# Performance work log

Measured on AMD Instinct MI355X. Metric: run time of the kernel, lower is better.

The kernel has to match this reference:

```python
import jax, jax.numpy as jnp
import numpy as np
from jax import lax

N_EMBD = 4096
N_EXPERTS = 64


def setup_inputs() -> dict:
    key = jax.random.key(0)
    kx, kw = jax.random.split(key)
    x = jax.random.normal(kx, (4, 4096, N_EMBD), dtype=jnp.float32)
    # nn.Linear(n_embd, n_experts, bias=False) -> weight shape [n_experts, n_embd]
    W = jax.random.normal(kw, (N_EXPERTS, N_EMBD), dtype=jnp.float32) * (1.0 / np.sqrt(N_EMBD))
    return {"x": x, "W": W}


def reference(x, W):
    # logits = x @ W^T : [B, S, n_experts]
    logits = jnp.einsum('bsd,ed->bse', x, W)
    topk_vals, topk_idx = lax.top_k(logits, 2)  # [B, S, 2]
    gates = jax.nn.softmax(topk_vals, axis=-1)  # softmax over just the top-2 values
    return (topk_idx, gates)
```

## Files before the change

kernel.cpp:

```cpp
#include <hip/hip_runtime.h>
#include <math.h>

#define N_EMBD    4096
#define N_EXPERTS 64
#define N_TOKENS  16384
#define TAU       1e-3f
#define BM        16
#define BK        128
#define NTILES    (N_EMBD / BK)

typedef __attribute__((ext_vector_type(8))) short bf16x8;
typedef __attribute__((ext_vector_type(4))) float f32x4;

#define MFMA16 __builtin_amdgcn_mfma_f32_16x16x32_bf16

struct hl_pair { unsigned h, l; };

__device__ __forceinline__ hl_pair split_pair(float f0, float f1) {
    unsigned u0 = __builtin_bit_cast(unsigned, f0);
    unsigned u1 = __builtin_bit_cast(unsigned, f1);
    unsigned r0 = u0 + 0x7FFFu + ((u0 >> 16) & 1u);
    unsigned r1 = u1 + 0x7FFFu + ((u1 >> 16) & 1u);
    hl_pair p;
    p.h = (r0 >> 16) | (r1 & 0xFFFF0000u);
    float h0 = __builtin_bit_cast(float, r0 & 0xFFFF0000u);
    float h1 = __builtin_bit_cast(float, r1 & 0xFFFF0000u);
    float l0 = f0 - h0;
    float l1 = f1 - h1;
    unsigned v0 = __builtin_bit_cast(unsigned, l0);
    unsigned v1 = __builtin_bit_cast(unsigned, l1);
    unsigned s0 = v0 + 0x7FFFu + ((v0 >> 16) & 1u);
    unsigned s1 = v1 + 0x7FFFu + ((v1 >> 16) & 1u);
    p.l = (s0 >> 16) | (s1 & 0xFFFF0000u);
    return p;
}

__global__ void w_pack_bf16(const float* __restrict__ W,
                            uint4* __restrict__ Bpack,
                            int* __restrict__ flags) {
    int tid = blockIdx.x * blockDim.x + threadIdx.x;
    if (tid == 0) flags[0] = 0;
    int lane = tid & 63;
    int nt   = (tid >> 6) & 3;
    int ks   = tid >> 8;
    int e = nt * 16 + (lane & 15);
    int k = ks * 32 + ((lane >> 4) << 3);
    const float* src = W + (size_t)e * N_EMBD + k;
    uint4 hp, lp;
    hl_pair p0 = split_pair(src[0], src[1]);
    hl_pair p1 = split_pair(src[2], src[3]);
    hl_pair p2 = split_pair(src[4], src[5]);
    hl_pair p3 = split_pair(src[6], src[7]);
    hp.x = p0.h; lp.x = p0.l;
    hp.y = p1.h; lp.y = p1.l;
    hp.z = p2.h; lp.z = p2.l;
    hp.w = p3.h; lp.w = p3.l;
    size_t F = (size_t)ks * 8 + nt * 2;
    Bpack[F * 64 + lane]       = hp;
    Bpack[(F + 1) * 64 + lane] = lp;
}

__device__ __forceinline__ void store_split(char* ldsA, int off, f32x4 v) {
    hl_pair p01 = split_pair(v.x, v.y);
    hl_pair p23 = split_pair(v.z, v.w);
    uint2 hw, lw;
    hw.x = p01.h; hw.y = p23.h;
    lw.x = p01.l; lw.y = p23.l;
    *(uint2*)(ldsA + off)        = hw;
    *(uint2*)(ldsA + off + 4096) = lw;
}

__global__ __launch_bounds__(256, 3) void router_fused(
        const float* __restrict__ x,
        const uint4* __restrict__ Bpack,
        float* __restrict__ out,
        int* __restrict__ flags) {
    __shared__ __align__(16) char ldsA[8192];
    __shared__ float red[BM][64];

    const int tid  = threadIdx.x;
    const int lane = tid & 63;
    const int w    = tid >> 6;
    const int tok0 = blockIdx.x * BM;

    const int k4   = tid & 31;
    const int row0 = tid >> 5;
    const f32x4* g0 = (const f32x4*)x + (size_t)(tok0 + row0) * (N_EMBD / 4) + k4;
    const f32x4* g1 = g0 + 8 * (N_EMBD / 4);
    const int swz = (row0 & 7) << 4;
    const int wo0 = ((row0    ) * 256 + k4 * 8) ^ swz;
    const int wo1 = ((row0 + 8) * 256 + k4 * 8) ^ swz;

    const int l15 = lane & 15, l16 = lane >> 4;
    const int ro_base = l15 * 256 + l16 * 16;
    const int swz_r   = (l15 & 7) << 4;

    f32x4 acc = {0.f, 0.f, 0.f, 0.f};

    f32x4 r0 = g0[0];
    f32x4 r1 = g1[0];
    for (int t = 0; t < NTILES; ++t) {
        __syncthreads();
        store_split(ldsA, wo0, r0);
        store_split(ldsA, wo1, r1);
        if (t + 1 < NTILES) {
            r0 = g0[(t + 1) * (BK / 4)];
            r1 = g1[(t + 1) * (BK / 4)];
        }
        __syncthreads();
#pragma unroll
        for (int ksl = 0; ksl < 4; ++ksl) {
            const uint4* bq = Bpack + ((size_t)(t * 4 + ksl) * 8 + w * 2) * 64 + lane;
            uint4 bhq = bq[0];
            uint4 blq = bq[64];
            const int off = (ro_base + ksl * 64) ^ swz_r;
            bf16x8 ah = *(const bf16x8*)(ldsA + off);
            bf16x8 al = *(const bf16x8*)(ldsA + off + 4096);
            bf16x8 bh = __builtin_bit_cast(bf16x8, bhq);
            bf16x8 bl = __builtin_bit_cast(bf16x8, blq);
            acc = MFMA16(ah, bh, acc, 0, 0, 0);
            acc = MFMA16(ah, bl, acc, 0, 0, 0);
            acc = MFMA16(al, bh, acc, 0, 0, 0);
        }
    }

    const int rb = l16 << 2;
#pragma unroll
    for (int j = 0; j < 4; ++j)
        red[rb + j][w * 16 + l15] = acc[j];
    __syncthreads();

    for (int tt = 0; tt < 4; ++tt) {
        const int t = w * 4 + tt;
        float v = red[t][lane];

        float m1 = v; int i1 = lane;
#pragma unroll
        for (int off = 32; off; off >>= 1) {
            float ov = __shfl_xor(m1, off); int oi = __shfl_xor(i1, off);
            if (ov > m1 || (ov == m1 && oi < i1)) { m1 = ov; i1 = oi; }
        }
        float m2 = (lane == i1) ? -INFINITY : v; int i2 = lane;
#pragma unroll
        for (int off = 32; off; off >>= 1) {
            float ov = __shfl_xor(m2, off); int oi = __shfl_xor(i2, off);
            if (ov > m2 || (ov == m2 && oi < i2)) { m2 = ov; i2 = oi; }
        }
        float m3 = (lane == i1 || lane == i2) ? -INFINITY : v;
#pragma unroll
        for (int off = 32; off; off >>= 1)
            m3 = fmaxf(m3, __shfl_xor(m3, off));

        if (lane == 0) {
            const int tok = tok0 + t;
            float e2  = __expf(m2 - m1);
            float inv = 1.0f / (1.0f + e2);
            float2 idx = make_float2((float)i1, (float)i2);
            float2 gts = make_float2(inv, e2 * inv);
            *(float2*)(out + 2 * tok) = idx;
            *(float2*)(out + 2 * N_TOKENS + 2 * tok) = gts;
            if ((m1 - m2 < TAU) || (m2 - m3 < TAU)) {
                int p = atomicAdd(flags, 1);
                if (p < N_TOKENS) flags[1 + p] = tok;
            }
        }
    }
}

__global__ __launch_bounds__(256) void refine(const float* __restrict__ x,
                                              const float* __restrict__ W,
                                              const int* __restrict__ flags,
                                              float* __restrict__ out) {
    __shared__ double redd[64];
    const int lane = threadIdx.x & 63;
    const int wv   = threadIdx.x >> 6;
    int cnt = flags[0];
    if (cnt > N_TOKENS) cnt = N_TOKENS;

    for (int i = blockIdx.x; i < cnt; i += gridDim.x) {
        const int tok = flags[1 + i];
        const float4* xr4 = (const float4*)(x + (size_t)tok * N_EMBD);
#pragma unroll
        for (int ee = 0; ee < 16; ++ee) {
            const int e = wv * 16 + ee;
            const float4* wr = (const float4*)(W + (size_t)e * N_EMBD);
            double acc = 0.0;
#pragma unroll 4
            for (int c = 0; c < 16; ++c) {
                float4 xv = xr4[c * 64 + lane];
                float4 wq = wr[c * 64 + lane];
                acc += (double)xv.x * wq.x + (double)xv.y * wq.y
                     + (double)xv.z * wq.z + (double)xv.w * wq.w;
            }
#pragma unroll
            for (int off = 32; off; off >>= 1)
                acc += __shfl_xor(acc, off);
            if (lane == 0) redd[e] = acc;
        }
        __syncthreads();
        if (wv == 0) {
            double v = redd[lane];
            double m1 = v; int i1 = lane;
#pragma unroll
            for (int off = 32; off; off >>= 1) {
                double ov = __shfl_xor(m1, off); int oi = __shfl_xor(i1, off);
                if (ov > m1 || (ov == m1 && oi < i1)) { m1 = ov; i1 = oi; }
            }
            double m2 = (lane == i1) ? -INFINITY : v; int i2 = lane;
#pragma unroll
            for (int off = 32; off; off >>= 1) {
                double ov = __shfl_xor(m2, off); int oi = __shfl_xor(i2, off);
                if (ov > m2 || (ov == m2 && oi < i2)) { m2 = ov; i2 = oi; }
            }
            if (lane == 0) {
                double e2  = exp(m2 - m1);
                double inv = 1.0 / (1.0 + e2);
                out[2 * tok + 0] = (float)i1;
                out[2 * tok + 1] = (float)i2;
                out[2 * N_TOKENS + 2 * tok + 0] = (float)inv;
                out[2 * N_TOKENS + 2 * tok + 1] = (float)(e2 * inv);
            }
        }
        __syncthreads();
    }
}

extern "C" void kernel_launch(void* const* d_in, const int* in_sizes, int n_in,
                              void* d_out, int out_size, void* d_ws, size_t ws_size,
                              hipStream_t stream) {
    const float* x = (const float*)d_in[0];
    const float* W = (const float*)d_in[1];
    float* out = (float*)d_out;

    uint4* Bpack = (uint4*)d_ws;
    int*   flags = (int*)((char*)d_ws + (2u << 20));

    w_pack_bf16 <<<128, 256, 0, stream>>>(W, Bpack, flags);
    router_fused<<<N_TOKENS / BM, 256, 0, stream>>>(x, Bpack, out, flags);
    refine      <<<128, 256, 0, stream>>>(x, W, flags, out);
}
```

Measured before the change: 110.8 us.

## Double-buffer LDS A tiles with one barrier per K step and deeper prefetch

Switches the A-tile staging in LDS to double buffering, so each K iteration needs one barrier instead of two. Global loads of x are now issued two tiles ahead, and all four B fragments per tile are loaded up front before the MFMAs. The occupancy hint rises from 3 to 4 blocks per CU. The cost is twice the LDS per block and more live registers, which may work against the higher occupancy target.

```diff
diff --git a/kernel.cpp b/kernel.cpp
--- a/kernel.cpp
+++ b/kernel.cpp
@@ -60,22 +60,22 @@
     Bpack[(F + 1) * 64 + lane] = lp;
 }
 
-__device__ __forceinline__ void store_split(char* ldsA, int off, f32x4 v) {
+__device__ __forceinline__ void store_split(char* buf, int off, f32x4 v) {
     hl_pair p01 = split_pair(v.x, v.y);
     hl_pair p23 = split_pair(v.z, v.w);
     uint2 hw, lw;
     hw.x = p01.h; hw.y = p23.h;
     lw.x = p01.l; lw.y = p23.l;
-    *(uint2*)(ldsA + off)        = hw;
-    *(uint2*)(ldsA + off + 4096) = lw;
-}
-
-__global__ __launch_bounds__(256, 3) void router_fused(
+    *(uint2*)(buf + off)        = hw;
+    *(uint2*)(buf + off + 4096) = lw;
+}
+
+__global__ __launch_bounds__(256, 4) void router_fused(
         const float* __restrict__ x,
         const uint4* __restrict__ Bpack,
         float* __restrict__ out,
         int* __restrict__ flags) {
-    __shared__ __align__(16) char ldsA[8192];
+    __shared__ __align__(16) char ldsA[2 * 8192];
     __shared__ float red[BM][64];
 
     const int tid  = threadIdx.x;
@@ -94,33 +94,65 @@
     const int l15 = lane & 15, l16 = lane >> 4;
     const int ro_base = l15 * 256 + l16 * 16;
     const int swz_r   = (l15 & 7) << 4;
+    const int off0 = (ro_base +   0) ^ swz_r;
+    const int off1 = (ro_base +  64) ^ swz_r;
+    const int off2 = (ro_base + 128) ^ swz_r;
+    const int off3 = (ro_base + 192) ^ swz_r;
 
     f32x4 acc = {0.f, 0.f, 0.f, 0.f};
 
     f32x4 r0 = g0[0];
     f32x4 r1 = g1[0];
+    store_split(ldsA, wo0, r0);
+    store_split(ldsA, wo1, r1);
+    r0 = g0[BK / 4];
+    r1 = g1[BK / 4];
+    asm volatile("s_waitcnt lgkmcnt(0)" ::: "memory");
+    __builtin_amdgcn_s_barrier();
+    __builtin_amdgcn_sched_barrier(0);
+
     for (int t = 0; t < NTILES; ++t) {
-        __syncthreads();
-        store_split(ldsA, wo0, r0);
-        store_split(ldsA, wo1, r1);
+        char* bufr = ldsA + (t & 1) * 8192;
+        char* bufw = ldsA + ((t & 1) ^ 1) * 8192;
+
+        const uint4* bq = Bpack + ((size_t)(t * 4) * 8 + w * 2) * 64 + lane;
+        uint4 bh0 = bq[0];    uint4 bl0 = bq[64];
+        uint4 bh1 = bq[512];  uint4 bl1 = bq[576];
+        uint4 bh2 = bq[1024]; uint4 bl2 = bq[1088];
+        uint4 bh3 = bq[1536]; uint4 bl3 = bq[1600];
+
+        bf16x8 ah, al;
+        ah = *(const bf16x8*)(bufr + off0);
+        al = *(const bf16x8*)(bufr + off0 + 4096);
+        acc = MFMA16(ah, __builtin_bit_cast(bf16x8, bh0), acc, 0, 0, 0);
+        acc = MFMA16(ah, __builtin_bit_cast(bf16x8, bl0), acc, 0, 0, 0);
+        acc = MFMA16(al, __builtin_bit_cast(bf16x8, bh0), acc, 0, 0, 0);
+        ah = *(const bf16x8*)(bufr + off1);
+        al = *(const bf16x8*)(bufr + off1 + 4096);
+        acc = MFMA16(ah, __builtin_bit_cast(bf16x8, bh1), acc, 0, 0, 0);
+        acc = MFMA16(ah, __builtin_bit_cast(bf16x8, bl1), acc, 0, 0, 0);
+        acc = MFMA16(al, __builtin_bit_cast(bf16x8, bh1), acc, 0, 0, 0);
+        ah = *(const bf16x8*)(bufr + off2);
+        al = *(const bf16x8*)(bufr + off2 + 4096);
+        acc = MFMA16(ah, __builtin_bit_cast(bf16x8, bh2), acc, 0, 0, 0);
+        acc = MFMA16(ah, __builtin_bit_cast(bf16x8, bl2), acc, 0, 0, 0);
+        acc = MFMA16(al, __builtin_bit_cast(bf16x8, bh2), acc, 0, 0, 0);
+        ah = *(const bf16x8*)(bufr + off3);
+        al = *(const bf16x8*)(bufr + off3 + 4096);
+        acc = MFMA16(ah, __builtin_bit_cast(bf16x8, bh3), acc, 0, 0, 0);
+        acc = MFMA16(ah, __builtin_bit_cast(bf16x8, bl3), acc, 0, 0, 0);
+        acc = MFMA16(al, __builtin_bit_cast(bf16x8, bh3), acc, 0, 0, 0);
+
         if (t + 1 < NTILES) {
-            r0 = g0[(t + 1) * (BK / 4)];
-            r1 = g1[(t + 1) * (BK / 4)];
-        }
-        __syncthreads();
-#pragma unroll
-        for (int ksl = 0; ksl < 4; ++ksl) {
-            const uint4* bq = Bpack + ((size_t)(t * 4 + ksl) * 8 + w * 2) * 64 + lane;
-            uint4 bhq = bq[0];
-            uint4 blq = bq[64];
-            const int off = (ro_base + ksl * 64) ^ swz_r;
-            bf16x8 ah = *(const bf16x8*)(ldsA + off);
-            bf16x8 al = *(const bf16x8*)(ldsA + off + 4096);
-            bf16x8 bh = __builtin_bit_cast(bf16x8, bhq);
-            bf16x8 bl = __builtin_bit_cast(bf16x8, blq);
-            acc = MFMA16(ah, bh, acc, 0, 0, 0);
-            acc = MFMA16(ah, bl, acc, 0, 0, 0);
-            acc = MFMA16(al, bh, acc, 0, 0, 0);
+            store_split(bufw, wo0, r0);
+            store_split(bufw, wo1, r1);
+            if (t + 2 < NTILES) {
+                r0 = g0[(t + 2) * (BK / 4)];
+                r1 = g1[(t + 2) * (BK / 4)];
+            }
+            asm volatile("s_waitcnt lgkmcnt(0)" ::: "memory");
+            __builtin_amdgcn_s_barrier();
+            __builtin_amdgcn_sched_barrier(0);
         }
     }
 
```

New measurement: 105.7 us. 1.05x faster.

## Double the token tile and double-buffer LDS with deeper register prefetch

Applied to the files above, without the earlier changes.

Raises the router tile from 16 to 32 tokens per block, so each block computes two MFMA accumulators per wave. This halves how often the packed bf16 hi/lo weights are re-read from cache across the grid. The A tile is now double-buffered in LDS, with one barrier per K tile instead of two, and x loads are prefetched two tiles ahead in registers. The cost is more registers and LDS, a launch bound lowered to 2 blocks per CU, and half as many blocks, which may reduce latency hiding for this memory-bound stream of x.

```diff
diff --git a/kernel.cpp b/kernel.cpp
--- a/kernel.cpp
+++ b/kernel.cpp
@@ -5,9 +5,11 @@
 #define N_EXPERTS 64
 #define N_TOKENS  16384
 #define TAU       1e-3f
-#define BM        16
+#define BM        32
 #define BK        128
 #define NTILES    (N_EMBD / BK)
+#define PLANE     8192
+#define BUFB      (2 * PLANE)
 
 typedef __attribute__((ext_vector_type(8))) short bf16x8;
 typedef __attribute__((ext_vector_type(4))) float f32x4;
@@ -60,78 +62,118 @@
     Bpack[(F + 1) * 64 + lane] = lp;
 }
 
-__device__ __forceinline__ void store_split(char* ldsA, int off, f32x4 v) {
+__device__ __forceinline__ void store_split(char* buf, int off, f32x4 v) {
     hl_pair p01 = split_pair(v.x, v.y);
     hl_pair p23 = split_pair(v.z, v.w);
     uint2 hw, lw;
     hw.x = p01.h; hw.y = p23.h;
     lw.x = p01.l; lw.y = p23.l;
-    *(uint2*)(ldsA + off)        = hw;
-    *(uint2*)(ldsA + off + 4096) = lw;
-}
-
-__global__ __launch_bounds__(256, 3) void router_fused(
+    *(uint2*)(buf + off)         = hw;
+    *(uint2*)(buf + off + PLANE) = lw;
+}
+
+__global__ __launch_bounds__(256, 2) void router_fused(
         const float* __restrict__ x,
         const uint4* __restrict__ Bpack,
         float* __restrict__ out,
         int* __restrict__ flags) {
-    __shared__ __align__(16) char ldsA[8192];
+    __shared__ __align__(16) char ldsA[2 * BUFB];
     __shared__ float red[BM][64];
 
     const int tid  = threadIdx.x;
     const int lane = tid & 63;
     const int w    = tid >> 6;
     const int tok0 = blockIdx.x * BM;
+    const int l15 = lane & 15, l16 = lane >> 4;
 
     const int k4   = tid & 31;
     const int row0 = tid >> 5;
-    const f32x4* g0 = (const f32x4*)x + (size_t)(tok0 + row0) * (N_EMBD / 4) + k4;
-    const f32x4* g1 = g0 + 8 * (N_EMBD / 4);
+    const f32x4* g0 = (const f32x4*)x + (size_t)(tok0 + row0     ) * (N_EMBD / 4) + k4;
+    const f32x4* g1 = (const f32x4*)x + (size_t)(tok0 + row0 +  8) * (N_EMBD / 4) + k4;
+    const f32x4* g2 = (const f32x4*)x + (size_t)(tok0 + row0 + 16) * (N_EMBD / 4) + k4;
+    const f32x4* g3 = (const f32x4*)x + (size_t)(tok0 + row0 + 24) * (N_EMBD / 4) + k4;
     const int swz = (row0 & 7) << 4;
-    const int wo0 = ((row0    ) * 256 + k4 * 8) ^ swz;
-    const int wo1 = ((row0 + 8) * 256 + k4 * 8) ^ swz;
-
-    const int l15 = lane & 15, l16 = lane >> 4;
-    const int ro_base = l15 * 256 + l16 * 16;
-    const int swz_r   = (l15 & 7) << 4;
-
-    f32x4 acc = {0.f, 0.f, 0.f, 0.f};
-
-    f32x4 r0 = g0[0];
-    f32x4 r1 = g1[0];
-    for (int t = 0; t < NTILES; ++t) {
-        __syncthreads();
-        store_split(ldsA, wo0, r0);
-        store_split(ldsA, wo1, r1);
-        if (t + 1 < NTILES) {
-            r0 = g0[(t + 1) * (BK / 4)];
-            r1 = g1[(t + 1) * (BK / 4)];
-        }
-        __syncthreads();
-#pragma unroll
-        for (int ksl = 0; ksl < 4; ++ksl) {
-            const uint4* bq = Bpack + ((size_t)(t * 4 + ksl) * 8 + w * 2) * 64 + lane;
-            uint4 bhq = bq[0];
-            uint4 blq = bq[64];
-            const int off = (ro_base + ksl * 64) ^ swz_r;
-            bf16x8 ah = *(const bf16x8*)(ldsA + off);
-            bf16x8 al = *(const bf16x8*)(ldsA + off + 4096);
-            bf16x8 bh = __builtin_bit_cast(bf16x8, bhq);
-            bf16x8 bl = __builtin_bit_cast(bf16x8, blq);
-            acc = MFMA16(ah, bh, acc, 0, 0, 0);
-            acc = MFMA16(ah, bl, acc, 0, 0, 0);
-            acc = MFMA16(al, bh, acc, 0, 0, 0);
-        }
-    }
-
-    const int rb = l16 << 2;
-#pragma unroll
-    for (int j = 0; j < 4; ++j)
-        red[rb + j][w * 16 + l15] = acc[j];
+    const int wo0 = (((row0     ) * 256) + k4 * 8) ^ swz;
+    const int wo1 = (((row0 +  8) * 256) + k4 * 8) ^ swz;
+    const int wo2 = (((row0 + 16) * 256) + k4 * 8) ^ swz;
+    const int wo3 = (((row0 + 24) * 256) + k4 * 8) ^ swz;
+
+    const int swz_r = (l15 & 7) << 4;
+    int ro[4];
+#pragma unroll
+    for (int ksl = 0; ksl < 4; ++ksl)
+        ro[ksl] = (l15 * 256 + l16 * 16 + ksl * 64) ^ swz_r;
+
+    f32x4 acc0 = {0.f, 0.f, 0.f, 0.f};
+    f32x4 acc1 = {0.f, 0.f, 0.f, 0.f};
+
+    f32x4 ra0, ra1, ra2, ra3, rb0, rb1, rb2, rb3;
+    char* buf0 = ldsA;
+    char* buf1 = ldsA + BUFB;
+
+#define LOADA(P, t) { P##0 = g0[(t) * 32]; P##1 = g1[(t) * 32];               \
+                      P##2 = g2[(t) * 32]; P##3 = g3[(t) * 32]; }
+#define STOREA(buf, P) { store_split(buf, wo0, P##0); store_split(buf, wo1, P##1); \
+                         store_split(buf, wo2, P##2); store_split(buf, wo3, P##3); }
+#define COMPUTE(bufR, tt) {                                                   \
+    const uint4* bq = Bpack + ((size_t)((tt) * 32 + w * 2)) * 64 + lane;      \
+    _Pragma("unroll")                                                         \
+    for (int ksl = 0; ksl < 4; ++ksl) {                                       \
+        uint4 bhq = bq[ksl * 512];                                            \
+        uint4 blq = bq[ksl * 512 + 64];                                       \
+        bf16x8 bh = __builtin_bit_cast(bf16x8, bhq);                          \
+        bf16x8 bl = __builtin_bit_cast(bf16x8, blq);                          \
+        bf16x8 ah0 = *(const bf16x8*)((bufR) + ro[ksl]);                      \
+        bf16x8 al0 = *(const bf16x8*)((bufR) + ro[ksl] + PLANE);              \
+        acc0 = MFMA16(ah0, bh, acc0, 0, 0, 0);                                \
+        acc0 = MFMA16(ah0, bl, acc0, 0, 0, 0);                                \
+        acc0 = MFMA16(al0, bh, acc0, 0, 0, 0);                                \
+        bf16x8 ah1 = *(const bf16x8*)((bufR) + ro[ksl] + 4096);               \
+        bf16x8 al1 = *(const bf16x8*)((bufR) + ro[ksl] + 4096 + PLANE);       \
+        acc1 = MFMA16(ah1, bh, acc1, 0, 0, 0);                                \
+        acc1 = MFMA16(ah1, bl, acc1, 0, 0, 0);                                \
+        acc1 = MFMA16(al1, bh, acc1, 0, 0, 0);                                \
+    } }
+
+    LOADA(rb, 0);
+    STOREA(buf0, rb);
+    LOADA(rb, 1);
+    LOADA(ra, 2);
+    asm volatile("s_waitcnt lgkmcnt(0)" ::: "memory");
+    __builtin_amdgcn_s_barrier();
+    __builtin_amdgcn_sched_barrier(0);
+
+    for (int t = 0; t < NTILES; t += 2) {
+        COMPUTE(buf0, t);
+        STOREA(buf1, rb);
+        asm volatile("s_waitcnt lgkmcnt(0)" ::: "memory");
+        __builtin_amdgcn_s_barrier();
+        __builtin_amdgcn_sched_barrier(0);
+
+        COMPUTE(buf1, t + 1);
+        if (t + 2 < NTILES) {
+            STOREA(buf0, ra);
+            if (t + 3 < NTILES) LOADA(rb, t + 3);
+            if (t + 4 < NTILES) LOADA(ra, t + 4);
+            asm volatile("s_waitcnt lgkmcnt(0)" ::: "memory");
+            __builtin_amdgcn_s_barrier();
+            __builtin_amdgcn_sched_barrier(0);
+        }
+    }
+#undef LOADA
+#undef STOREA
+#undef COMPUTE
+
+    const int rb_ = l16 << 2;
+#pragma unroll
+    for (int j = 0; j < 4; ++j) {
+        red[rb_ + j][w * 16 + l15]      = acc0[j];
+        red[16 + rb_ + j][w * 16 + l15] = acc1[j];
+    }
     __syncthreads();
 
-    for (int tt = 0; tt < 4; ++tt) {
-        const int t = w * 4 + tt;
+    for (int tt = 0; tt < 8; ++tt) {
+        const int t = w * 8 + tt;
         float v = red[t][lane];
 
         float m1 = v; int i1 = lane;
```

Measured after the change: 136.7 us. 23.4% more time.
